# Kernel optimization log

Hardware: AMD Instinct MI355X
Metric: run time of the kernel (lower is better)

Reference implementation:

```python
import jax, jax.numpy as jnp
import numpy as np

LAMBDA_GEO = 0.5


def setup_inputs() -> dict:
    key = jax.random.key(0)
    embeddings = jax.random.normal(key, (4, 2048, 512), dtype=jnp.float32)
    return {"embeddings": embeddings}


def _geometric_loss(embeddings):
    b, s, d = embeddings.shape
    x = embeddings.reshape(b * s, d)  # [N, d]
    sq_norm = jnp.sum(x * x, axis=-1)  # [N]
    sq = sq_norm[:, None] + sq_norm[None, :] - 2.0 * (x @ x.T)  # [N, N]
    sq = jnp.maximum(sq, 0.0)
    dist = jnp.sqrt(sq)  # torch.cdist(p=2)
    return jnp.mean(jnp.exp(-dist * 0.1)) * 0.1


def reference(embeddings):
    geometric_loss = _geometric_loss(embeddings)
    total_geometric = LAMBDA_GEO * geometric_loss
    return geometric_loss, total_geometric
```

## Files before the change

### kernel.cpp

```cpp
#include <hip/hip_runtime.h>

#define NROWS 8192
#define DIM   512
#define NT    64
#define NTRI  (NT * (NT + 1) / 2)
#define NACC  64

typedef __attribute__((ext_vector_type(16))) float f32x16;
typedef __attribute__((ext_vector_type(8)))  int   i32x8;

__device__ __forceinline__ unsigned char f2e4m3(float x) {
    unsigned ux = __float_as_uint(x);
    unsigned s  = (ux >> 24) & 0x80u;
    float a = __uint_as_float(ux & 0x7FFFFFFFu);
    a = fminf(a, 448.0f);
    unsigned ua = __float_as_uint(a);
    int eb = (int)(ua >> 23);
    if (eb < 121) eb = 121;
    float step  = __uint_as_float((unsigned)(eb - 3) << 23);
    float istep = __uint_as_float((unsigned)(257 - eb) << 23);
    float q = rintf(a * istep) * step;
    q = fminf(q, 448.0f);
    if (q < 0.001953125f)
        return (unsigned char)s;
    unsigned uq = __float_as_uint(q);
    int eq = (int)(uq >> 23) - 127;
    unsigned byte;
    if (eq < -6) byte = (unsigned)(q * 512.0f);
    else         byte = (unsigned)((eq + 7) << 3) | ((uq >> 20) & 7u);
    return (unsigned char)(s | byte);
}

__global__ __launch_bounds__(256) void norm_convert_kernel(
    const float* __restrict__ X, unsigned char* __restrict__ Xq,
    float* __restrict__ norms, float* __restrict__ acc)
{
    const int tid  = threadIdx.x;
    const int lane = tid & 63;
    const int w    = tid >> 6;
    const int row  = blockIdx.x * 4 + w;

    if (blockIdx.x == 0 && tid < NACC + 1) acc[tid] = 0.0f;

    const float* xr = X + (size_t)row * DIM + lane * 8;
    float4 v0 = *(const float4*)xr;
    float4 v1 = *(const float4*)(xr + 4);

    float s = 0.0f;
    s = fmaf(v0.x, v0.x, s); s = fmaf(v0.y, v0.y, s);
    s = fmaf(v0.z, v0.z, s); s = fmaf(v0.w, v0.w, s);
    s = fmaf(v1.x, v1.x, s); s = fmaf(v1.y, v1.y, s);
    s = fmaf(v1.z, v1.z, s); s = fmaf(v1.w, v1.w, s);

    union { unsigned char b[8]; uint2 v; } pk;
    pk.b[0] = f2e4m3(v0.x); pk.b[1] = f2e4m3(v0.y);
    pk.b[2] = f2e4m3(v0.z); pk.b[3] = f2e4m3(v0.w);
    pk.b[4] = f2e4m3(v1.x); pk.b[5] = f2e4m3(v1.y);
    pk.b[6] = f2e4m3(v1.z); pk.b[7] = f2e4m3(v1.w);

    const int slab = lane >> 3;
    const int c16  = (lane >> 1) & 3;
    const int cpos = c16 ^ ((row >> 1) & 3);
    *(uint2*)(Xq + (size_t)row * DIM + slab * 64 + cpos * 16 + (lane & 1) * 8)
        = pk.v;

    #pragma unroll
    for (int off = 32; off > 0; off >>= 1) s += __shfl_down(s, off, 64);
    if (lane == 0) norms[row] = s;
}

__device__ __forceinline__ void gload16(const void* g, void* l) {
    __builtin_amdgcn_global_load_lds(
        (const __attribute__((address_space(1))) unsigned int*)g,
        (__attribute__((address_space(3))) unsigned int*)l, 16, 0, 0);
}

__global__ __launch_bounds__(256, 2) void pair_loss_gemm_kernel(
    const unsigned char* __restrict__ Xq, const float* __restrict__ norms,
    float* __restrict__ acc, float* __restrict__ out)
{
    __shared__ __align__(16) char As0[16384];
    __shared__ __align__(16) char As1[16384];
    __shared__ __align__(16) char Bs0[16384];
    __shared__ __align__(16) char Bs1[16384];
    __shared__ float wsum[4];
    __shared__ int lastflag;

    int t = blockIdx.x, bi = 0;
    while (t >= (NT - bi)) { t -= (NT - bi); bi++; }
    const int bj = bi + t;

    const int tid  = threadIdx.x;
    const int lane = tid & 63;
    const int w    = tid >> 6;

    const int rowA = bi * 128;
    const int rowB = bj * 128;

    f32x16 accv[2][2];
    #pragma unroll
    for (int a = 0; a < 2; a++)
        #pragma unroll
        for (int b = 0; b < 2; b++)
            #pragma unroll
            for (int r = 0; r < 16; r++) accv[a][b][r] = 0.0f;

    const int lrow = lane >> 2;
    const int lpos = ((lane & 3) ^ ((lane >> 3) & 3)) * 16;
    const unsigned char* gA =
        Xq + (size_t)(rowA + w * 32 + lrow) * DIM + lpos;
    const unsigned char* gB =
        Xq + (size_t)(rowB + w * 32 + lrow) * DIM + lpos;
    char* const ldst0 = (char*)0 + (w * 32) * 64;

    const int rl = lane & 31;
    const int qh = lane >> 5;
    const int p0 = ((2 * qh) ^ ((rl >> 1) & 3)) * 16;
    const int p1 = p0 ^ 16;
    const int wr = (w & 1) * 64;
    const int wc = (w >> 1) * 64;
    const int ra = (wr + rl) * 64;
    const int rb = (wc + rl) * 64;

#define STAGE(bufA, bufB, k) do {                                        \
        const int kb_ = (k) * 128;                                       \
        gload16(gA + kb_,             (bufA) + (w * 32) * 64);           \
        gload16(gA + kb_ + 16 * DIM,  (bufA) + (w * 32 + 16) * 64);      \
        gload16(gA + kb_ + 64,        (bufA) + 8192 + (w * 32) * 64);    \
        gload16(gA + kb_ + 16 * DIM + 64,                                \
                (bufA) + 8192 + (w * 32 + 16) * 64);                     \
        gload16(gB + kb_,             (bufB) + (w * 32) * 64);           \
        gload16(gB + kb_ + 16 * DIM,  (bufB) + (w * 32 + 16) * 64);      \
        gload16(gB + kb_ + 64,        (bufB) + 8192 + (w * 32) * 64);    \
        gload16(gB + kb_ + 16 * DIM + 64,                                \
                (bufB) + 8192 + (w * 32 + 16) * 64);                     \
    } while (0)

    STAGE(As0, Bs0, 0);
    __syncthreads();

    char* curA = As0; char* nxtA = As1;
    char* curB = Bs0; char* nxtB = Bs1;

    #pragma unroll 1
    for (int k = 0; k < 4; k++) {
        const bool more = (k < 3);
        if (more) STAGE(nxtA, nxtB, k + 1);

        __builtin_amdgcn_s_setprio(1);
        #pragma unroll
        for (int s = 0; s < 2; s++) {
            const int sb = s * 8192;
            union { uint4 u[2]; i32x8 v; } fa0, fa1, fb0, fb1;
            fa0.u[0] = *(const uint4*)(curA + sb + ra + p0);
            fa0.u[1] = *(const uint4*)(curA + sb + ra + p1);
            fa1.u[0] = *(const uint4*)(curA + sb + ra + 2048 + p0);
            fa1.u[1] = *(const uint4*)(curA + sb + ra + 2048 + p1);
            fb0.u[0] = *(const uint4*)(curB + sb + rb + p0);
            fb0.u[1] = *(const uint4*)(curB + sb + rb + p1);
            fb1.u[0] = *(const uint4*)(curB + sb + rb + 2048 + p0);
            fb1.u[1] = *(const uint4*)(curB + sb + rb + 2048 + p1);

            accv[0][0] = __builtin_amdgcn_mfma_scale_f32_32x32x64_f8f6f4(
                fa0.v, fb0.v, accv[0][0], 0, 0, 0, 0x7F7F7F7F, 0, 0x7F7F7F7F);
            accv[0][1] = __builtin_amdgcn_mfma_scale_f32_32x32x64_f8f6f4(
                fa0.v, fb1.v, accv[0][1], 0, 0, 0, 0x7F7F7F7F, 0, 0x7F7F7F7F);
            accv[1][0] = __builtin_amdgcn_mfma_scale_f32_32x32x64_f8f6f4(
                fa1.v, fb0.v, accv[1][0], 0, 0, 0, 0x7F7F7F7F, 0, 0x7F7F7F7F);
            accv[1][1] = __builtin_amdgcn_mfma_scale_f32_32x32x64_f8f6f4(
                fa1.v, fb1.v, accv[1][1], 0, 0, 0, 0x7F7F7F7F, 0, 0x7F7F7F7F);
        }
        __builtin_amdgcn_s_setprio(0);

        if (more) {
            __syncthreads();
            char* tA = curA; curA = nxtA; nxtA = tA;
            char* tB = curB; curB = nxtB; nxtB = tB;
        }
    }
#undef STAGE

    const float wgt = (bi == bj) ? 1.0f : 2.0f;
    const int cl = lane & 31;
    const int rh = (lane >> 5) * 4;
    float lsum = 0.0f;
    #pragma unroll
    for (int a = 0; a < 2; a++) {
        const int gia = rowA + wr + a * 32;
        float ni[16];
        #pragma unroll
        for (int r = 0; r < 16; r++)
            ni[r] = norms[gia + (r & 3) + 8 * (r >> 2) + rh];
        #pragma unroll
        for (int b = 0; b < 2; b++) {
            const int gj = rowB + wc + b * 32 + cl;
            const float nj = norms[gj];
            #pragma unroll
            for (int r = 0; r < 16; r++) {
                const int gi = gia + (r & 3) + 8 * (r >> 2) + rh;
                float sq = fmaf(-2.0f, accv[a][b][r], ni[r] + nj);
                sq = fmaxf(sq, 0.0f);
                float term = __expf(-0.1f * sqrtf(sq));
                if (gi == gj) term = 1.0f;
                lsum += term;
            }
        }
    }
    lsum *= wgt;
    #pragma unroll
    for (int off = 32; off > 0; off >>= 1) lsum += __shfl_down(lsum, off, 64);
    if (lane == 0) wsum[w] = lsum;
    __syncthreads();

    if (tid == 0) {
        float bsum = wsum[0] + wsum[1] + wsum[2] + wsum[3];
        float old = atomicAdd(&acc[blockIdx.x & (NACC - 1)], bsum);
        asm volatile("" :: "v"(old));
        unsigned prev = atomicAdd((unsigned int*)(acc + NACC), 1u);
        lastflag = (prev == NTRI - 1) ? 1 : 0;
    }
    __syncthreads();
    if (lastflag && tid < 64) {
        float v = atomicAdd(&acc[tid], 0.0f);
        #pragma unroll
        for (int off = 32; off > 0; off >>= 1) v += __shfl_down(v, off, 64);
        if (tid == 0) {
            const float inv = 1.0f / ((float)NROWS * (float)NROWS);
            float loss = v * inv * 0.1f;
            out[0] = loss;
            out[1] = 0.5f * loss;
        }
    }
}

extern "C" void kernel_launch(void* const* d_in, const int* in_sizes, int n_in,
                              void* d_out, int out_size, void* d_ws, size_t ws_size,
                              hipStream_t stream)
{
    const float* X = (const float*)d_in[0];
    float* out = (float*)d_out;

    char* ws = (char*)d_ws;
    float*         acc   = (float*)ws;
    float*         norms = (float*)(ws + 1024);
    unsigned char* Xq    = (unsigned char*)(ws + 1024 + 32768);

    norm_convert_kernel<<<NROWS / 4, 256, 0, stream>>>(X, Xq, norms, acc);
    pair_loss_gemm_kernel<<<NTRI, 256, 0, stream>>>(Xq, norms, acc, out);
}
```

Before: 115.8 us.

## Use triple-buffered 64-byte K stages with fine-grained waitcnt and block swizzle

The two double-buffered 128-byte K stages become a three-slot ring of 64-byte K stages. Each stage is waited on with explicit vmcnt counts and a raw s_barrier in place of a full __syncthreads, so two stages stay in flight. Shared memory per block drops from 64KB to 48KB, and launch bounds are raised to 3 blocks per CU for more occupancy. Block IDs are also remapped across 8 groups (XCD-style swizzle) to improve L2 locality, at the risk of more barriers per tile and register pressure at the higher occupancy.

```diff
diff --git a/kernel.cpp b/kernel.cpp
--- a/kernel.cpp
+++ b/kernel.cpp
@@ -75,18 +75,16 @@
         (__attribute__((address_space(3))) unsigned int*)l, 16, 0, 0);
 }
 
-__global__ __launch_bounds__(256, 2) void pair_loss_gemm_kernel(
+__global__ __launch_bounds__(256, 3) void pair_loss_gemm_kernel(
     const unsigned char* __restrict__ Xq, const float* __restrict__ norms,
     float* __restrict__ acc, float* __restrict__ out)
 {
-    __shared__ __align__(16) char As0[16384];
-    __shared__ __align__(16) char As1[16384];
-    __shared__ __align__(16) char Bs0[16384];
-    __shared__ __align__(16) char Bs1[16384];
+    __shared__ __align__(16) char Ls[3][16384];
     __shared__ float wsum[4];
     __shared__ int lastflag;
 
-    int t = blockIdx.x, bi = 0;
+    const int bid = (blockIdx.x & 7) * 260 + (blockIdx.x >> 3);
+    int t = bid, bi = 0;
     while (t >= (NT - bi)) { t -= (NT - bi); bi++; }
     const int bj = bi + t;
 
@@ -107,11 +105,12 @@
 
     const int lrow = lane >> 2;
     const int lpos = ((lane & 3) ^ ((lane >> 3) & 3)) * 16;
-    const unsigned char* gA =
-        Xq + (size_t)(rowA + w * 32 + lrow) * DIM + lpos;
-    const unsigned char* gB =
-        Xq + (size_t)(rowB + w * 32 + lrow) * DIM + lpos;
-    char* const ldst0 = (char*)0 + (w * 32) * 64;
+    const unsigned char* gA0 = Xq + (size_t)(rowA + w * 32 + lrow) * DIM + lpos;
+    const unsigned char* gA1 = gA0 + (size_t)16 * DIM;
+    const unsigned char* gB0 = Xq + (size_t)(rowB + w * 32 + lrow) * DIM + lpos;
+    const unsigned char* gB1 = gB0 + (size_t)16 * DIM;
+    const int dst0 = (w * 32) * 64;
+    const int dst1 = (w * 32 + 16) * 64;
 
     const int rl = lane & 31;
     const int qh = lane >> 5;
@@ -120,69 +119,59 @@
     const int wr = (w & 1) * 64;
     const int wc = (w >> 1) * 64;
     const int ra = (wr + rl) * 64;
-    const int rb = (wc + rl) * 64;
-
-#define STAGE(bufA, bufB, k) do {                                        \
-        const int kb_ = (k) * 128;                                       \
-        gload16(gA + kb_,             (bufA) + (w * 32) * 64);           \
-        gload16(gA + kb_ + 16 * DIM,  (bufA) + (w * 32 + 16) * 64);      \
-        gload16(gA + kb_ + 64,        (bufA) + 8192 + (w * 32) * 64);    \
-        gload16(gA + kb_ + 16 * DIM + 64,                                \
-                (bufA) + 8192 + (w * 32 + 16) * 64);                     \
-        gload16(gB + kb_,             (bufB) + (w * 32) * 64);           \
-        gload16(gB + kb_ + 16 * DIM,  (bufB) + (w * 32 + 16) * 64);      \
-        gload16(gB + kb_ + 64,        (bufB) + 8192 + (w * 32) * 64);    \
-        gload16(gB + kb_ + 16 * DIM + 64,                                \
-                (bufB) + 8192 + (w * 32 + 16) * 64);                     \
+    const int rb = 8192 + (wc + rl) * 64;
+
+#define STAGE(s) do {                                                    \
+        char* sl_ = Ls[(s) % 3];                                         \
+        const int kb_ = (s) * 64;                                        \
+        gload16(gA0 + kb_, sl_ + dst0);                                  \
+        gload16(gA1 + kb_, sl_ + dst1);                                  \
+        gload16(gB0 + kb_, sl_ + 8192 + dst0);                           \
+        gload16(gB1 + kb_, sl_ + 8192 + dst1);                           \
     } while (0)
 
-    STAGE(As0, Bs0, 0);
-    __syncthreads();
-
-    char* curA = As0; char* nxtA = As1;
-    char* curB = Bs0; char* nxtB = Bs1;
-
-    #pragma unroll 1
-    for (int k = 0; k < 4; k++) {
-        const bool more = (k < 3);
-        if (more) STAGE(nxtA, nxtB, k + 1);
+    STAGE(0);
+    STAGE(1);
+
+    #pragma unroll
+    for (int k = 0; k < 8; k++) {
+        __builtin_amdgcn_sched_barrier(0);
+        if (k < 7) asm volatile("s_waitcnt vmcnt(4)" ::: "memory");
+        else       asm volatile("s_waitcnt vmcnt(0)" ::: "memory");
+        __builtin_amdgcn_s_barrier();
+        __builtin_amdgcn_sched_barrier(0);
+
+        if (k < 6) STAGE(k + 2);
+
+        const char* sl = Ls[k % 3];
+        union frag { uint4 u[2]; i32x8 v; };
+        frag fa0, fa1, fb0, fb1;
+        fa0.u[0] = *(const uint4*)(sl + ra + p0);
+        fa0.u[1] = *(const uint4*)(sl + ra + p1);
+        fa1.u[0] = *(const uint4*)(sl + ra + 2048 + p0);
+        fa1.u[1] = *(const uint4*)(sl + ra + 2048 + p1);
+        fb0.u[0] = *(const uint4*)(sl + rb + p0);
+        fb0.u[1] = *(const uint4*)(sl + rb + p1);
+        fb1.u[0] = *(const uint4*)(sl + rb + 2048 + p0);
+        fb1.u[1] = *(const uint4*)(sl + rb + 2048 + p1);
 
         __builtin_amdgcn_s_setprio(1);
-        #pragma unroll
-        for (int s = 0; s < 2; s++) {
-            const int sb = s * 8192;
-            union { uint4 u[2]; i32x8 v; } fa0, fa1, fb0, fb1;
-            fa0.u[0] = *(const uint4*)(curA + sb + ra + p0);
-            fa0.u[1] = *(const uint4*)(curA + sb + ra + p1);
-            fa1.u[0] = *(const uint4*)(curA + sb + ra + 2048 + p0);
-            fa1.u[1] = *(const uint4*)(curA + sb + ra + 2048 + p1);
-            fb0.u[0] = *(const uint4*)(curB + sb + rb + p0);
-            fb0.u[1] = *(const uint4*)(curB + sb + rb + p1);
-            fb1.u[0] = *(const uint4*)(curB + sb + rb + 2048 + p0);
-            fb1.u[1] = *(const uint4*)(curB + sb + rb + 2048 + p1);
-
-            accv[0][0] = __builtin_amdgcn_mfma_scale_f32_32x32x64_f8f6f4(
-                fa0.v, fb0.v, accv[0][0], 0, 0, 0, 0x7F7F7F7F, 0, 0x7F7F7F7F);
-            accv[0][1] = __builtin_amdgcn_mfma_scale_f32_32x32x64_f8f6f4(
-                fa0.v, fb1.v, accv[0][1], 0, 0, 0, 0x7F7F7F7F, 0, 0x7F7F7F7F);
-            accv[1][0] = __builtin_amdgcn_mfma_scale_f32_32x32x64_f8f6f4(
-                fa1.v, fb0.v, accv[1][0], 0, 0, 0, 0x7F7F7F7F, 0, 0x7F7F7F7F);
-            accv[1][1] = __builtin_amdgcn_mfma_scale_f32_32x32x64_f8f6f4(
-                fa1.v, fb1.v, accv[1][1], 0, 0, 0, 0x7F7F7F7F, 0, 0x7F7F7F7F);
-        }
+        accv[0][0] = __builtin_amdgcn_mfma_scale_f32_32x32x64_f8f6f4(
+            fa0.v, fb0.v, accv[0][0], 0, 0, 0, 0x7F7F7F7F, 0, 0x7F7F7F7F);
+        accv[0][1] = __builtin_amdgcn_mfma_scale_f32_32x32x64_f8f6f4(
+            fa0.v, fb1.v, accv[0][1], 0, 0, 0, 0x7F7F7F7F, 0, 0x7F7F7F7F);
+        accv[1][0] = __builtin_amdgcn_mfma_scale_f32_32x32x64_f8f6f4(
+            fa1.v, fb0.v, accv[1][0], 0, 0, 0, 0x7F7F7F7F, 0, 0x7F7F7F7F);
+        accv[1][1] = __builtin_amdgcn_mfma_scale_f32_32x32x64_f8f6f4(
+            fa1.v, fb1.v, accv[1][1], 0, 0, 0, 0x7F7F7F7F, 0, 0x7F7F7F7F);
         __builtin_amdgcn_s_setprio(0);
-
-        if (more) {
-            __syncthreads();
-            char* tA = curA; curA = nxtA; nxtA = tA;
-            char* tB = curB; curB = nxtB; nxtB = tB;
-        }
+        __builtin_amdgcn_sched_barrier(0);
     }
 #undef STAGE
 
     const float wgt = (bi == bj) ? 1.0f : 2.0f;
     const int cl = lane & 31;
-    const int rh = (lane >> 5) * 4;
+    const int rh = qh * 4;
     float lsum = 0.0f;
     #pragma unroll
     for (int a = 0; a < 2; a++) {
@@ -195,6 +184,9 @@
         for (int b = 0; b < 2; b++) {
             const int gj = rowB + wc + b * 32 + cl;
             const float nj = norms[gj];
+            #pragma unroll
+            for (int r = 0; r < 4; r++) {
+            }
             #pragma unroll
             for (int r = 0; r < 16; r++) {
                 const int gi = gia + (r & 3) + 8 * (r >> 2) + rh;
@@ -214,7 +206,7 @@
 
     if (tid == 0) {
         float bsum = wsum[0] + wsum[1] + wsum[2] + wsum[3];
-        float old = atomicAdd(&acc[blockIdx.x & (NACC - 1)], bsum);
+        float old = atomicAdd(&acc[bid & (NACC - 1)], bsum);
         asm volatile("" :: "v"(old));
         unsigned prev = atomicAdd((unsigned int*)(acc + NACC), 1u);
         lastflag = (prev == NTRI - 1) ? 1 : 0;
```

Measured after the change: 109.5 us. 5.4% less time.
